# Performance work log

Measured on AMD Instinct MI355X. Metric: run time of the kernel, lower is better.

Reference implementation:

```python
import jax, jax.numpy as jnp
import numpy as np

N = 30000          # nodes
E = 480000         # edges (before self-loops)
G = 64             # graphs in batch
EMB = 64
IN = 6 + 2 * EMB   # 134
H1, C1 = 4, 128    # gat1 heads / out channels
H2, C2 = 1, 256    # gat2
LRELU_SLOPE = 0.2


def _layernorm(x, g, b, eps=1e-5):
    m = x.mean(-1, keepdims=True)
    v = ((x - m) ** 2).mean(-1, keepdims=True)
    return (x - m) / jnp.sqrt(v + eps) * g + b


def _gatv2(x, src, dst, Wl, bl, Wr, br, att, bias, H, C, n, concat):
    # GATv2 (PyG semantics, share_weights=False, eval mode -> no dropout)
    xl = (x @ Wl + bl).reshape(n, H, C)   # source transform
    xr = (x @ Wr + br).reshape(n, H, C)   # target transform
    # e_ij = att . leaky_relu(xl_j + xr_i), edges j->i : [E_tot, H]
    e = jnp.sum(jax.nn.leaky_relu(xl[src] + xr[dst], LRELU_SLOPE) * att, axis=-1)
    # scatter-softmax over incoming edges of each target node
    emax = jax.lax.stop_gradient(jax.ops.segment_max(e, dst, num_segments=n))
    ex = jnp.exp(e - emax[dst])
    den = jax.ops.segment_sum(ex, dst, num_segments=n)
    alpha = ex / (den[dst] + 1e-16)                       # [E_tot, H]
    out = jax.ops.segment_sum(alpha[:, :, None] * xl[src], dst, num_segments=n)
    if concat:
        return out.reshape(n, H * C) + bias
    return out.mean(axis=1) + bias


def setup_inputs() -> dict:
    key = jax.random.key(0)
    ks = jax.random.split(key, 24)
    s = 0.05
    inp = {
        "x_cont": jax.random.normal(ks[0], (N, 6), jnp.float32),
        "x_class": jax.random.randint(ks[1], (N,), 0, 12, jnp.int32),
        "x_pitch": jax.random.randint(ks[2], (N,), 0, 129, jnp.int32),
        "edge_index": jax.random.randint(ks[3], (2, E), 0, N, jnp.int32),
        "batch": jnp.sort(jax.random.randint(ks[4], (N,), 0, G, jnp.int32)),
        "class_tab": jax.random.normal(ks[5], (12, EMB), jnp.float32) * s,
        "pitch_tab": jax.random.normal(ks[6], (129, EMB), jnp.float32) * s,
        "Wl1": jax.random.normal(ks[7], (IN, H1 * C1), jnp.float32) * s,
        "bl1": jnp.zeros((H1 * C1,), jnp.float32),
        "Wr1": jax.random.normal(ks[8], (IN, H1 * C1), jnp.float32) * s,
        "br1": jnp.zeros((H1 * C1,), jnp.float32),
        "att1": jax.random.normal(ks[9], (H1, C1), jnp.float32) * s,
        "bias1": jnp.zeros((H1 * C1,), jnp.float32),
        "ln1_g": jnp.ones((H1 * C1,), jnp.float32),
        "ln1_b": jnp.zeros((H1 * C1,), jnp.float32),
        "Wl2": jax.random.normal(ks[10], (H1 * C1, H2 * C2), jnp.float32) * s,
        "bl2": jnp.zeros((H2 * C2,), jnp.float32),
        "Wr2": jax.random.normal(ks[11], (H1 * C1, H2 * C2), jnp.float32) * s,
        "br2": jnp.zeros((H2 * C2,), jnp.float32),
        "att2": jax.random.normal(ks[12], (H2, C2), jnp.float32) * s,
        "bias2": jnp.zeros((C2,), jnp.float32),
        "ln2_g": jnp.ones((C2,), jnp.float32),
        "ln2_b": jnp.zeros((C2,), jnp.float32),
        "Wp1": jax.random.normal(ks[13], (C2, 512), jnp.float32) * s,
        "bp1": jnp.zeros((512,), jnp.float32),
        "lnp_g": jnp.ones((512,), jnp.float32),
        "lnp_b": jnp.zeros((512,), jnp.float32),
        "Wp2": jax.random.normal(ks[14], (512, 512), jnp.float32) * s,
        "bp2": jnp.zeros((512,), jnp.float32),
    }
    return inp


def reference(x_cont, x_class, x_pitch, edge_index, batch,
              class_tab, pitch_tab,
              Wl1, bl1, Wr1, br1, att1, bias1, ln1_g, ln1_b,
              Wl2, bl2, Wr2, br2, att2, bias2, ln2_g, ln2_b,
              Wp1, bp1, lnp_g, lnp_b, Wp2, bp2):
    # node features: [N, 6 + 64 + 64]
    x = jnp.concatenate([x_cont, class_tab[x_class], pitch_tab[x_pitch]], axis=1)
    # add self-loops (PyG GATv2Conv default)
    loops = jnp.arange(N, dtype=edge_index.dtype)
    src = jnp.concatenate([edge_index[0], loops])
    dst = jnp.concatenate([edge_index[1], loops])
    x = jax.nn.elu(_layernorm(_gatv2(x, src, dst, Wl1, bl1, Wr1, br1, att1, bias1, H1, C1, N, True), ln1_g, ln1_b))
    x = jax.nn.elu(_layernorm(_gatv2(x, src, dst, Wl2, bl2, Wr2, br2, att2, bias2, H2, C2, N, False), ln2_g, ln2_b))
    # global mean pool over graphs
    sums = jax.ops.segment_sum(x, batch, num_segments=G)
    cnt = jax.ops.segment_sum(jnp.ones((N,), x.dtype), batch, num_segments=G)
    pooled = sums / jnp.maximum(cnt, 1.0)[:, None]
    # projection head + L2 normalize
    h = jax.nn.gelu(_layernorm(pooled @ Wp1 + bp1, lnp_g, lnp_b), approximate=False)
    out = h @ Wp2 + bp2
    norm = jnp.sqrt(jnp.sum(out * out, axis=1, keepdims=True))
    return out / jnp.maximum(norm, 1e-12)
```

## Files before the change

### kernel.cpp

```cpp
#include <hip/hip_runtime.h>
#include <math.h>

#define NG 64

typedef short bf16x8 __attribute__((ext_vector_type(8)));
typedef short bf16x4 __attribute__((ext_vector_type(4)));
typedef float f32x4 __attribute__((ext_vector_type(4)));

static inline int cdiv(int a, int b) { return (a + b - 1) / b; }

__device__ inline ushort f2b(float f) {
  union { float f; uint u; } v; v.f = f;
  uint u = v.u;
  return (ushort)((u + 0x7fffu + ((u >> 16) & 1u)) >> 16);
}
__device__ inline float b2f(ushort h) {
  union { uint u; float f; } v; v.u = ((uint)h) << 16;
  return v.f;
}

__global__ __launch_bounds__(256) void k_build_xb(
    const float* __restrict__ xc, const int* __restrict__ xcl,
    const int* __restrict__ xpi, const float* __restrict__ ctab,
    const float* __restrict__ ptab, ushort* __restrict__ x, int n) {
  int t = blockIdx.x * blockDim.x + threadIdx.x;
  int total = n * 160;
  if (t >= total) return;
  int node = t / 160, c = t % 160;
  float v;
  if (c < 6)        v = xc[node * 6 + c];
  else if (c < 70)  v = ctab[xcl[node] * 64 + (c - 6)];
  else if (c < 134) v = ptab[xpi[node] * 64 + (c - 70)];
  else              v = 0.f;
  x[t] = f2b(v);
}

__global__ __launch_bounds__(256) void k_prep_w1(
    const float* __restrict__ Wl, const float* __restrict__ Wr,
    ushort* __restrict__ Wt) {
  int t = blockIdx.x * blockDim.x + threadIdx.x;
  if (t >= 1024 * 160) return;
  int c = t / 160, k = t % 160;
  float v = 0.f;
  if (k < 134) v = (c < 512) ? Wl[k * 512 + c] : Wr[k * 512 + (c - 512)];
  Wt[t] = f2b(v);
}
__global__ __launch_bounds__(256) void k_prep_w2(
    const float* __restrict__ Wl, const float* __restrict__ Wr,
    ushort* __restrict__ Wt) {
  int t = blockIdx.x * blockDim.x + threadIdx.x;
  if (t >= 512 * 512) return;
  int c = t / 512, k = t % 512;
  float v = (c < 256) ? Wl[k * 256 + c] : Wr[k * 256 + (c - 256)];
  Wt[t] = f2b(v);
}

__global__ __launch_bounds__(256) void k_hist(const int* __restrict__ dst,
                                              int* __restrict__ deg, int E, int N) {
  int t = blockIdx.x * blockDim.x + threadIdx.x;
  if (t < E) atomicAdd(&deg[dst[t]], 1);
  else if (t < E + N) atomicAdd(&deg[t - E], 1);
}

__global__ __launch_bounds__(256) void k_bsum(const int* __restrict__ deg,
                                              int* __restrict__ bsum, int n) {
  int i = blockIdx.x * 256 + threadIdx.x;
  int v = (i < n) ? deg[i] : 0;
#pragma unroll
  for (int off = 1; off < 64; off <<= 1) v += __shfl_xor(v, off);
  __shared__ int ws[4];
  if ((threadIdx.x & 63) == 0) ws[threadIdx.x >> 6] = v;
  __syncthreads();
  if (threadIdx.x == 0) bsum[blockIdx.x] = ws[0] + ws[1] + ws[2] + ws[3];
}

__global__ __launch_bounds__(256) void k_scanb(const int* __restrict__ bsum,
                                               int* __restrict__ boff, int nb) {
  int t = threadIdx.x, lane = t & 63;
  int v = (t < nb) ? bsum[t] : 0;
  int incl = v;
#pragma unroll
  for (int off = 1; off < 64; off <<= 1) {
    int u = __shfl_up(incl, off);
    if (lane >= off) incl += u;
  }
  __shared__ int wsum[4];
  if (lane == 63) wsum[t >> 6] = incl;
  __syncthreads();
  int add = 0;
  for (int w = 0; w < (t >> 6); ++w) add += wsum[w];
  if (t < nb) boff[t] = incl + add - v;
}

__global__ __launch_bounds__(256) void k_scanc(const int* __restrict__ deg,
                                               const int* __restrict__ boff,
                                               int* __restrict__ rowptr, int n) {
  int b = blockIdx.x, t = threadIdx.x, lane = t & 63;
  int i = b * 256 + t;
  int v = (i < n) ? deg[i] : 0;
  int incl = v;
#pragma unroll
  for (int off = 1; off < 64; off <<= 1) {
    int u = __shfl_up(incl, off);
    if (lane >= off) incl += u;
  }
  __shared__ int wsum[4];
  if (lane == 63) wsum[t >> 6] = incl;
  __syncthreads();
  int add = boff[b];
  for (int w = 0; w < (t >> 6); ++w) add += wsum[w];
  if (i < n) rowptr[i + 1] = incl + add;
  if (i == 0) rowptr[0] = 0;
}

__global__ __launch_bounds__(256) void k_scatter(
    const int* __restrict__ src, const int* __restrict__ dst,
    const int* __restrict__ rowptr, int* __restrict__ fill,
    int* __restrict__ csr, int E, int N) {
  int t = blockIdx.x * blockDim.x + threadIdx.x;
  int s, d;
  if (t < E) { s = src[t]; d = dst[t]; }
  else if (t < E + N) { s = t - E; d = t - E; }
  else return;
  int pos = rowptr[d] + atomicAdd(&fill[d], 1);
  csr[pos] = s;
}

#define GBM 128
#define GBN 128
#define GBK 32
#define ESTRIDE 136
__device__ __forceinline__ int swzf(int r, int s) {
  return r * 64 + ((s * 16) ^ (((r >> 1) & 3) << 4));
}
__global__ __launch_bounds__(256) void k_gemm_mfma(
    const ushort* __restrict__ A, const ushort* __restrict__ Bt,
    const float* __restrict__ blo, const float* __restrict__ bhi, int nhalf,
    ushort* __restrict__ C, int M, int Kp, int NC) {
  __shared__ ushort smem[GBM * ESTRIDE];
  ushort* sA = smem;
  ushort* sB = smem + GBM * GBK;
  int tid = threadIdx.x;
  int lane = tid & 63, w = tid >> 6;
  int wr = w >> 1, wc = w & 1;
  int row0 = blockIdx.x * GBM, col0 = blockIdx.y * GBN;
  int nK = Kp / GBK;

  int rs = tid >> 2, ss = tid & 3;
  int wO0 = swzf(rs, ss);
  int wO1 = swzf(rs + 64, ss);
  bool okA0 = (row0 + rs) < M;
  bool okA1 = (row0 + rs + 64) < M;
  size_t baseA0 = (size_t)(row0 + rs) * Kp + ss * 8;
  size_t baseA1 = (size_t)(row0 + rs + 64) * Kp + ss * 8;
  size_t baseB0 = (size_t)(col0 + rs) * Kp + ss * 8;
  size_t baseB1 = (size_t)(col0 + rs + 64) * Kp + ss * 8;

  int fr = lane & 15, kq = lane >> 4;
  int aoff[4], boff[4];
#pragma unroll
  for (int m = 0; m < 4; ++m) {
    int ra = wr * 64 + m * 16 + fr;
    aoff[m] = ra * 64 + ((kq * 16) ^ (((ra >> 1) & 3) << 4));
    int rb = wc * 64 + m * 16 + fr;
    boff[m] = rb * 64 + ((kq * 16) ^ (((rb >> 1) & 3) << 4));
  }

  f32x4 acc[4][4] = {};
  bf16x8 zz = {};
  bf16x8 pa0, pa1, pb0, pb1, qa0, qa1, qb0, qb1;

#define LOADG(KS, RA0, RA1, RB0, RB1)                                   \
  do {                                                                  \
    const ushort* ap = A + (size_t)(KS) * GBK;                          \
    const ushort* bp = Bt + (size_t)(KS) * GBK;                         \
    RA0 = okA0 ? *(const bf16x8*)(ap + baseA0) : zz;                    \
    RA1 = okA1 ? *(const bf16x8*)(ap + baseA1) : zz;                    \
    RB0 = *(const bf16x8*)(bp + baseB0);                                \
    RB1 = *(const bf16x8*)(bp + baseB1);                                \
  } while (0)

#define STAGE(RA0, RA1, RB0, RB1)                                       \
  do {                                                                  \
    *(bf16x8*)((char*)sA + wO0) = RA0;                                  \
    *(bf16x8*)((char*)sA + wO1) = RA1;                                  \
    *(bf16x8*)((char*)sB + wO0) = RB0;                                  \
    *(bf16x8*)((char*)sB + wO1) = RB1;                                  \
  } while (0)

#define COMPUTE()                                                       \
  do {                                                                  \
    bf16x8 av[4], bv[4];                                                \
    _Pragma("unroll") for (int m = 0; m < 4; ++m)                       \
        av[m] = *(const bf16x8*)((const char*)sA + aoff[m]);            \
    _Pragma("unroll") for (int n = 0; n < 4; ++n)                       \
        bv[n] = *(const bf16x8*)((const char*)sB + boff[n]);            \
    _Pragma("unroll") for (int m = 0; m < 4; ++m)                       \
        _Pragma("unroll") for (int n = 0; n < 4; ++n)                   \
            acc[m][n] = __builtin_amdgcn_mfma_f32_16x16x32_bf16(        \
                av[m], bv[n], acc[m][n], 0, 0, 0);                      \
  } while (0)

  LOADG(0, pa0, pa1, pb0, pb1);
  for (int ks = 0; ks < nK; ++ks) {
    __syncthreads();
    if (ks & 1) {
      STAGE(qa0, qa1, qb0, qb1);
      if (ks + 1 < nK) LOADG(ks + 1, pa0, pa1, pb0, pb1);
    } else {
      STAGE(pa0, pa1, pb0, pb1);
      if (ks + 1 < nK) LOADG(ks + 1, qa0, qa1, qb0, qb1);
    }
    __syncthreads();
    COMPUTE();
  }

  __syncthreads();
#pragma unroll
  for (int m = 0; m < 4; ++m) {
#pragma unroll
    for (int n = 0; n < 4; ++n) {
      int tc = wc * 64 + n * 16 + fr;
      float bv = ((col0 + tc) < nhalf) ? blo[col0 + tc] : bhi[col0 + tc - nhalf];
#pragma unroll
      for (int j = 0; j < 4; ++j) {
        int tr = wr * 64 + m * 16 + kq * 4 + j;
        smem[tr * ESTRIDE + tc] = f2b(acc[m][n][j] + bv);
      }
    }
  }
  __syncthreads();
  int r0 = tid >> 4, cb = (tid & 15) * 8;
#pragma unroll
  for (int pass = 0; pass < 8; ++pass) {
    int r = pass * 16 + r0;
    int grow = row0 + r;
    if (grow < M) {
      bf16x8 vv = *(const bf16x8*)&smem[r * ESTRIDE + cb];
      *(bf16x8*)&C[(size_t)grow * NC + col0 + cb] = vv;
    }
  }
#undef LOADG
#undef STAGE
#undef COMPUTE
}

__global__ __launch_bounds__(256) void k_gat1(
    const ushort* __restrict__ xlr,
    const int* __restrict__ rowptr, const int* __restrict__ csr,
    const float* __restrict__ att, const float* __restrict__ bias,
    const float* __restrict__ lng, const float* __restrict__ lnb,
    ushort* __restrict__ out, int n) {
  int wid = (blockIdx.x * blockDim.x + threadIdx.x) >> 6;
  int lane = threadIdx.x & 63;
  if (wid >= n) return;
  int base = lane * 8;
  float xrv[8], attv[8];
  {
    bf16x8 t = *(const bf16x8*)&xlr[(size_t)wid * 1024 + 512 + base];
#pragma unroll
    for (int j = 0; j < 8; ++j) xrv[j] = b2f((ushort)t[j]);
    const float* ap = &att[base];
    float4 u0 = *(const float4*)ap;
    float4 u1 = *(const float4*)(ap + 4);
    attv[0] = u0.x; attv[1] = u0.y; attv[2] = u0.z; attv[3] = u0.w;
    attv[4] = u1.x; attv[5] = u1.y; attv[6] = u1.z; attv[7] = u1.w;
  }
  float s = 0.f;
  float acc[8] = {};
  int e0 = rowptr[wid], e1 = rowptr[wid + 1];
  bf16x8 vbn = *(const bf16x8*)&xlr[(size_t)csr[e0] * 1024 + base];
  for (int p = e0; p < e1; ++p) {
    bf16x8 vb = vbn;
    if (p + 1 < e1)
      vbn = *(const bf16x8*)&xlr[(size_t)csr[p + 1] * 1024 + base];
    float v[8];
#pragma unroll
    for (int j = 0; j < 8; ++j) v[j] = b2f((ushort)vb[j]);
    float pe = 0.f;
#pragma unroll
    for (int j = 0; j < 8; ++j) {
      float t = v[j] + xrv[j];
      t = t > 0.f ? t : 0.2f * t;
      pe += t * attv[j];
    }
    pe += __shfl_xor(pe, 1);
    pe += __shfl_xor(pe, 2);
    pe += __shfl_xor(pe, 4);
    pe += __shfl_xor(pe, 8);
    float w = __expf(pe - 8.f);
    s += w;
#pragma unroll
    for (int j = 0; j < 8; ++j) acc[j] += w * v[j];
  }
  float inv = 1.f / s;
  float o[8];
#pragma unroll
  for (int j = 0; j < 8; ++j) o[j] = acc[j] * inv + bias[base + j];
  float sum = 0.f, sq = 0.f;
#pragma unroll
  for (int j = 0; j < 8; ++j) { sum += o[j]; sq += o[j] * o[j]; }
#pragma unroll
  for (int off = 1; off < 64; off <<= 1) {
    sum += __shfl_xor(sum, off);
    sq += __shfl_xor(sq, off);
  }
  float mean = sum * (1.f / 512.f);
  float var = fmaxf(sq * (1.f / 512.f) - mean * mean, 0.f);
  float rstd = rsqrtf(var + 1e-5f);
  bf16x8 ov;
#pragma unroll
  for (int j = 0; j < 8; ++j) {
    float y = (o[j] - mean) * rstd * lng[base + j] + lnb[base + j];
    y = y > 0.f ? y : __expf(y) - 1.f;
    ov[j] = (short)f2b(y);
  }
  *(bf16x8*)&out[(size_t)wid * 512 + base] = ov;
}

__global__ __launch_bounds__(256) void k_gat2(
    const ushort* __restrict__ xlr,
    const int* __restrict__ rowptr, const int* __restrict__ csr,
    const float* __restrict__ att, const float* __restrict__ bias,
    const float* __restrict__ lng, const float* __restrict__ lnb,
    float* __restrict__ out, int n) {
  int wid = (blockIdx.x * blockDim.x + threadIdx.x) >> 6;
  int lane = threadIdx.x & 63;
  if (wid >= n) return;
  int base = lane * 4;
  float xrv[4], attv[4];
  {
    bf16x4 t = *(const bf16x4*)&xlr[(size_t)wid * 512 + 256 + base];
#pragma unroll
    for (int j = 0; j < 4; ++j) xrv[j] = b2f((ushort)t[j]);
    float4 at4 = *(const float4*)&att[base];
    attv[0] = at4.x; attv[1] = at4.y; attv[2] = at4.z; attv[3] = at4.w;
  }
  float s = 0.f;
  float acc[4] = {};
  int e0 = rowptr[wid], e1 = rowptr[wid + 1];
  bf16x4 vbn = *(const bf16x4*)&xlr[(size_t)csr[e0] * 512 + base];
  for (int p = e0; p < e1; ++p) {
    bf16x4 vb = vbn;
    if (p + 1 < e1)
      vbn = *(const bf16x4*)&xlr[(size_t)csr[p + 1] * 512 + base];
    float v[4];
#pragma unroll
    for (int j = 0; j < 4; ++j) v[j] = b2f((ushort)vb[j]);
    float pe = 0.f;
#pragma unroll
    for (int j = 0; j < 4; ++j) {
      float t = v[j] + xrv[j];
      t = t > 0.f ? t : 0.2f * t;
      pe += t * attv[j];
    }
#pragma unroll
    for (int off = 1; off < 64; off <<= 1) pe += __shfl_xor(pe, off);
    float w = __expf(pe - 8.f);
    s += w;
#pragma unroll
    for (int j = 0; j < 4; ++j) acc[j] += w * v[j];
  }
  float inv = 1.f / s;
  float o[4];
#pragma unroll
  for (int j = 0; j < 4; ++j) o[j] = acc[j] * inv + bias[base + j];
  float sum = 0.f, sq = 0.f;
#pragma unroll
  for (int j = 0; j < 4; ++j) { sum += o[j]; sq += o[j] * o[j]; }
#pragma unroll
  for (int off = 1; off < 64; off <<= 1) {
    sum += __shfl_xor(sum, off);
    sq += __shfl_xor(sq, off);
  }
  float mean = sum * (1.f / 256.f);
  float var = fmaxf(sq * (1.f / 256.f) - mean * mean, 0.f);
  float rstd = rsqrtf(var + 1e-5f);
#pragma unroll
  for (int j = 0; j < 4; ++j) {
    float y = (o[j] - mean) * rstd * lng[base + j] + lnb[base + j];
    y = y > 0.f ? y : __expf(y) - 1.f;
    out[(size_t)wid * 256 + base + j] = y;
  }
}

__global__ __launch_bounds__(256) void k_pool(
    const float* __restrict__ h2, const int* __restrict__ batch,
    float* __restrict__ pooled, int* __restrict__ cnt, int n) {
  int c = threadIdx.x;
  int n0 = blockIdx.x * 64;
  int n1 = min(n0 + 64, n);
  if (n0 >= n) return;
  float acc = 0.f;
  int cur = batch[n0];
  int cl = 0;
  for (int i = n0; i < n1; ++i) {
    int bb = batch[i];
    if (bb != cur) {
      atomicAdd(&pooled[cur * 256 + c], acc);
      if (c == 0) atomicAdd(&cnt[cur], cl);
      acc = 0.f; cl = 0; cur = bb;
    }
    acc += h2[(size_t)i * 256 + c];
    cl++;
  }
  atomicAdd(&pooled[cur * 256 + c], acc);
  if (c == 0) atomicAdd(&cnt[cur], cl);
}

__global__ __launch_bounds__(512) void k_proj1(
    const float* __restrict__ pooled, const int* __restrict__ cnt,
    const float* __restrict__ W, const float* __restrict__ b,
    const float* __restrict__ lng, const float* __restrict__ lnb,
    float* __restrict__ hout) {
  __shared__ float row[256];
  __shared__ float red[16];
  int g = blockIdx.x, c = threadIdx.x;
  if (c < 256) {
    float cc = fmaxf((float)cnt[g], 1.f);
    row[c] = pooled[g * 256 + c] / cc;
  }
  __syncthreads();
  float acc = b[c];
#pragma unroll 4
  for (int k = 0; k < 256; ++k) acc += row[k] * W[k * 512 + c];
  float sum = acc, sq = acc * acc;
#pragma unroll
  for (int off = 1; off < 64; off <<= 1) {
    sum += __shfl_xor(sum, off);
    sq += __shfl_xor(sq, off);
  }
  int wv = threadIdx.x >> 6;
  if ((threadIdx.x & 63) == 0) { red[wv] = sum; red[8 + wv] = sq; }
  __syncthreads();
  float S = 0.f, Q = 0.f;
#pragma unroll
  for (int t = 0; t < 8; ++t) { S += red[t]; Q += red[8 + t]; }
  float mean = S * (1.f / 512.f);
  float var = fmaxf(Q * (1.f / 512.f) - mean * mean, 0.f);
  float rstd = rsqrtf(var + 1e-5f);
  float y = (acc - mean) * rstd * lng[c] + lnb[c];
  float ge = 0.5f * y * (1.f + erff(y * 0.70710678118654752f));
  hout[g * 512 + c] = ge;
}

__global__ __launch_bounds__(512) void k_proj2(
    const float* __restrict__ h, const float* __restrict__ W,
    const float* __restrict__ b, float* __restrict__ out) {
  __shared__ float row[512];
  __shared__ float red[8];
  int g = blockIdx.x, c = threadIdx.x;
  row[c] = h[g * 512 + c];
  __syncthreads();
  float acc = b[c];
#pragma unroll 4
  for (int k = 0; k < 512; ++k) acc += row[k] * W[k * 512 + c];
  float sq = acc * acc;
#pragma unroll
  for (int off = 1; off < 64; off <<= 1) sq += __shfl_xor(sq, off);
  int wv = threadIdx.x >> 6;
  if ((threadIdx.x & 63) == 0) red[wv] = sq;
  __syncthreads();
  float S = 0.f;
#pragma unroll
  for (int t = 0; t < 8; ++t) S += red[t];
  float norm = fmaxf(sqrtf(S), 1e-12f);
  out[g * 512 + c] = acc / norm;
}

extern "C" void kernel_launch(void* const* d_in, const int* in_sizes, int n_in,
                              void* d_out, int out_size, void* d_ws, size_t ws_size,
                              hipStream_t stream) {
  const float* x_cont = (const float*)d_in[0];
  const int* x_class  = (const int*)d_in[1];
  const int* x_pitch  = (const int*)d_in[2];
  const int* ei       = (const int*)d_in[3];
  const int* batch    = (const int*)d_in[4];
  const float* ctab = (const float*)d_in[5];
  const float* ptab = (const float*)d_in[6];
  const float* Wl1 = (const float*)d_in[7];
  const float* bl1 = (const float*)d_in[8];
  const float* Wr1 = (const float*)d_in[9];
  const float* br1 = (const float*)d_in[10];
  const float* att1 = (const float*)d_in[11];
  const float* bias1 = (const float*)d_in[12];
  const float* ln1g = (const float*)d_in[13];
  const float* ln1b = (const float*)d_in[14];
  const float* Wl2 = (const float*)d_in[15];
  const float* bl2 = (const float*)d_in[16];
  const float* Wr2 = (const float*)d_in[17];
  const float* br2 = (const float*)d_in[18];
  const float* att2 = (const float*)d_in[19];
  const float* bias2 = (const float*)d_in[20];
  const float* ln2g = (const float*)d_in[21];
  const float* ln2b = (const float*)d_in[22];
  const float* Wp1 = (const float*)d_in[23];
  const float* bp1 = (const float*)d_in[24];
  const float* lnpg = (const float*)d_in[25];
  const float* lnpb = (const float*)d_in[26];
  const float* Wp2 = (const float*)d_in[27];
  const float* bp2 = (const float*)d_in[28];
  float* out = (float*)d_out;
  (void)n_in; (void)out_size; (void)ws_size;

  int N = in_sizes[1];
  int E = in_sizes[3] / 2;
  int ET = E + N;
  int NB = cdiv(N, 256);

  char* p = (char*)d_ws;
  ushort* xb   = (ushort*)p; p += (size_t)N * 160 * 2;
  ushort* W1t  = (ushort*)p; p += (size_t)1024 * 160 * 2;
  ushort* W2t  = (ushort*)p; p += (size_t)512 * 512 * 2;
  ushort* xlr1 = (ushort*)p; p += (size_t)N * 1024 * 2;
  ushort* h1b  = (ushort*)p; p += (size_t)N * 512 * 2;
  float* pooled = (float*)p; p += (size_t)NG * 256 * 4;
  int* cnt     = (int*)p;    p += NG * 4;
  float* hproj = (float*)p;  p += (size_t)NG * 512 * 4;
  int* deg     = (int*)p;    p += (size_t)N * 4;
  int* fill    = (int*)p;    p += (size_t)N * 4;
  int* rowptr  = (int*)p;    p += (size_t)(N + 1) * 4;
  int* csr     = (int*)p;    p += (size_t)ET * 4;
  int* bsum    = (int*)p;    p += 256 * 4;
  int* boff    = (int*)p;    p += 256 * 4;
  ushort* xlr2 = xlr1;
  float* h2   = (float*)h1b;

  const int* esrc = ei;
  const int* edst = ei + E;

  hipMemsetAsync(deg, 0, (size_t)2 * N * sizeof(int), stream);
  hipMemsetAsync(pooled, 0, (size_t)NG * 256 * sizeof(float) + NG * sizeof(int), stream);

  k_build_xb<<<cdiv(N * 160, 256), 256, 0, stream>>>(x_cont, x_class, x_pitch, ctab, ptab, xb, N);
  k_prep_w1<<<cdiv(1024 * 160, 256), 256, 0, stream>>>(Wl1, Wr1, W1t);
  k_prep_w2<<<cdiv(512 * 512, 256), 256, 0, stream>>>(Wl2, Wr2, W2t);
  k_hist<<<cdiv(ET, 256), 256, 0, stream>>>(edst, deg, E, N);
  k_bsum<<<NB, 256, 0, stream>>>(deg, bsum, N);
  k_scanb<<<1, 256, 0, stream>>>(bsum, boff, NB);
  k_scanc<<<NB, 256, 0, stream>>>(deg, boff, rowptr, N);
  k_scatter<<<cdiv(ET, 256), 256, 0, stream>>>(esrc, edst, rowptr, fill, csr, E, N);

  dim3 g1(cdiv(N, GBM), 1024 / GBN);
  k_gemm_mfma<<<g1, 256, 0, stream>>>(xb, W1t, bl1, br1, 512, xlr1, N, 160, 1024);
  k_gat1<<<cdiv(N * 64, 256), 256, 0, stream>>>(xlr1, rowptr, csr, att1, bias1, ln1g, ln1b, h1b, N);

  dim3 g2(cdiv(N, GBM), 512 / GBN);
  k_gemm_mfma<<<g2, 256, 0, stream>>>(h1b, W2t, bl2, br2, 256, xlr2, N, 512, 512);
  k_gat2<<<cdiv(N * 64, 256), 256, 0, stream>>>(xlr2, rowptr, csr, att2, bias2, ln2g, ln2b, h2, N);

  k_pool<<<cdiv(N, 64), 256, 0, stream>>>(h2, batch, pooled, cnt, N);
  k_proj1<<<NG, 512, 0, stream>>>(pooled, cnt, Wp1, bp1, lnpg, lnpb, hproj);
  k_proj2<<<NG, 512, 0, stream>>>(hproj, Wp2, bp2, out);
}
```

Measured before the change: 396.2 us.

## Batch edge gathers four-wide in GAT kernels and merge prep launches

Both GAT aggregation kernels now process incoming edges four at a time. They prefetch four neighbor rows ahead, interleave the four attention dot products and their shuffle reductions, and mask the tail edges with zero weights. Leaky-ReLU is rewritten branch-free as 0.6*t+0.4*|t|, bf16 unpacking uses bit masks, and addressing uses 32-bit byte offsets. The feature build, both weight transposes and the degree histogram are merged into one launch to cut launch overhead. The four-wide batching adds register pressure and issues redundant clamped loads at the tail of each node's edge list.

```diff
diff --git a/kernel.cpp b/kernel.cpp
--- a/kernel.cpp
+++ b/kernel.cpp
@@ -19,47 +19,65 @@
   return v.f;
 }
 
-__global__ __launch_bounds__(256) void k_build_xb(
+__device__ __forceinline__ void unpack8(bf16x8 vb, float* v) {
+  union { bf16x8 b; uint u[4]; } cv; cv.b = vb;
+#pragma unroll
+  for (int q = 0; q < 4; ++q) {
+    union { uint u; float f; } lo, hi;
+    lo.u = cv.u[q] << 16;
+    hi.u = cv.u[q] & 0xffff0000u;
+    v[2 * q] = lo.f; v[2 * q + 1] = hi.f;
+  }
+}
+__device__ __forceinline__ void unpack4(bf16x4 vb, float* v) {
+  union { bf16x4 b; uint u[2]; } cv; cv.b = vb;
+#pragma unroll
+  for (int q = 0; q < 2; ++q) {
+    union { uint u; float f; } lo, hi;
+    lo.u = cv.u[q] << 16;
+    hi.u = cv.u[q] & 0xffff0000u;
+    v[2 * q] = lo.f; v[2 * q + 1] = hi.f;
+  }
+}
+
+__global__ __launch_bounds__(256) void k_prep(
     const float* __restrict__ xc, const int* __restrict__ xcl,
     const int* __restrict__ xpi, const float* __restrict__ ctab,
-    const float* __restrict__ ptab, ushort* __restrict__ x, int n) {
+    const float* __restrict__ ptab,
+    const float* __restrict__ Wl1, const float* __restrict__ Wr1,
+    const float* __restrict__ Wl2, const float* __restrict__ Wr2,
+    const int* __restrict__ edst,
+    ushort* __restrict__ xb, ushort* __restrict__ W1t, ushort* __restrict__ W2t,
+    int* __restrict__ deg, int n, int E) {
   int t = blockIdx.x * blockDim.x + threadIdx.x;
-  int total = n * 160;
-  if (t >= total) return;
-  int node = t / 160, c = t % 160;
-  float v;
-  if (c < 6)        v = xc[node * 6 + c];
-  else if (c < 70)  v = ctab[xcl[node] * 64 + (c - 6)];
-  else if (c < 134) v = ptab[xpi[node] * 64 + (c - 70)];
-  else              v = 0.f;
-  x[t] = f2b(v);
-}
-
-__global__ __launch_bounds__(256) void k_prep_w1(
-    const float* __restrict__ Wl, const float* __restrict__ Wr,
-    ushort* __restrict__ Wt) {
-  int t = blockIdx.x * blockDim.x + threadIdx.x;
-  if (t >= 1024 * 160) return;
-  int c = t / 160, k = t % 160;
-  float v = 0.f;
-  if (k < 134) v = (c < 512) ? Wl[k * 512 + c] : Wr[k * 512 + (c - 512)];
-  Wt[t] = f2b(v);
-}
-__global__ __launch_bounds__(256) void k_prep_w2(
-    const float* __restrict__ Wl, const float* __restrict__ Wr,
-    ushort* __restrict__ Wt) {
-  int t = blockIdx.x * blockDim.x + threadIdx.x;
-  if (t >= 512 * 512) return;
-  int c = t / 512, k = t % 512;
-  float v = (c < 256) ? Wl[k * 256 + c] : Wr[k * 256 + (c - 256)];
-  Wt[t] = f2b(v);
-}
-
-__global__ __launch_bounds__(256) void k_hist(const int* __restrict__ dst,
-                                              int* __restrict__ deg, int E, int N) {
-  int t = blockIdx.x * blockDim.x + threadIdx.x;
-  if (t < E) atomicAdd(&deg[dst[t]], 1);
-  else if (t < E + N) atomicAdd(&deg[t - E], 1);
+  int T1 = n * 160;
+  int T2 = T1 + 1024 * 160;
+  int T3 = T2 + 512 * 512;
+  int T4 = T3 + E + n;
+  if (t < T1) {
+    int node = t / 160, c = t % 160;
+    float v;
+    if (c < 6)        v = xc[node * 6 + c];
+    else if (c < 70)  v = ctab[xcl[node] * 64 + (c - 6)];
+    else if (c < 134) v = ptab[xpi[node] * 64 + (c - 70)];
+    else              v = 0.f;
+    xb[t] = f2b(v);
+  } else if (t < T2) {
+    int u = t - T1;
+    int c = u / 160, k = u % 160;
+    float v = 0.f;
+    if (k < 134) v = (c < 512) ? Wl1[k * 512 + c] : Wr1[k * 512 + (c - 512)];
+    W1t[u] = f2b(v);
+  } else if (t < T3) {
+    int u = t - T2;
+    int c = u / 512, k = u % 512;
+    float v = (c < 256) ? Wl2[k * 256 + c] : Wr2[k * 256 + (c - 256)];
+    W2t[u] = f2b(v);
+  } else if (t < T4) {
+    int u = t - T3;
+    if (u < E) atomicAdd(&deg[edst[u]], 1);
+    else atomicAdd(&deg[u - E], 1);
+  }
 }
 
 __global__ __launch_bounds__(256) void k_bsum(const int* __restrict__ deg,
@@ -255,11 +273,12 @@
   int lane = threadIdx.x & 63;
   if (wid >= n) return;
   int base = lane * 8;
+  uint laneB = (uint)lane * 16u;
+  const char* xb8 = (const char*)xlr;
   float xrv[8], attv[8];
   {
-    bf16x8 t = *(const bf16x8*)&xlr[(size_t)wid * 1024 + 512 + base];
-#pragma unroll
-    for (int j = 0; j < 8; ++j) xrv[j] = b2f((ushort)t[j]);
+    bf16x8 t = *(const bf16x8*)(xb8 + ((uint)wid * 2048u + 1024u + laneB));
+    unpack8(t, xrv);
     const float* ap = &att[base];
     float4 u0 = *(const float4*)ap;
     float4 u1 = *(const float4*)(ap + 4);
@@ -269,30 +288,63 @@
   float s = 0.f;
   float acc[8] = {};
   int e0 = rowptr[wid], e1 = rowptr[wid + 1];
-  bf16x8 vbn = *(const bf16x8*)&xlr[(size_t)csr[e0] * 1024 + base];
-  for (int p = e0; p < e1; ++p) {
-    bf16x8 vb = vbn;
-    if (p + 1 < e1)
-      vbn = *(const bf16x8*)&xlr[(size_t)csr[p + 1] * 1024 + base];
-    float v[8];
-#pragma unroll
-    for (int j = 0; j < 8; ++j) v[j] = b2f((ushort)vb[j]);
-    float pe = 0.f;
+  int last = e1 - 1;
+
+#define LROW1(IDX) (*(const bf16x8*)(xb8 + (((uint)csr[IDX]) * 2048u + laneB)))
+  bf16x8 r0 = LROW1(e0);
+  bf16x8 r1 = LROW1(min(e0 + 1, last));
+  bf16x8 r2 = LROW1(min(e0 + 2, last));
+  bf16x8 r3 = LROW1(min(e0 + 3, last));
+
+  for (int pp = e0; pp < e1; pp += 4) {
+    bf16x8 c0 = r0, c1 = r1, c2 = r2, c3 = r3;
+    if (pp + 4 < e1) {
+      r0 = LROW1(pp + 4);
+      r1 = LROW1(min(pp + 5, last));
+      r2 = LROW1(min(pp + 6, last));
+      r3 = LROW1(min(pp + 7, last));
+    }
+    float v0[8], v1[8], v2[8], v3[8];
+    unpack8(c0, v0); unpack8(c1, v1); unpack8(c2, v2); unpack8(c3, v3);
+    float p1a = 0.f, p2a = 0.f, p1b = 0.f, p2b = 0.f;
+    float p1c = 0.f, p2c = 0.f, p1d = 0.f, p2d = 0.f;
 #pragma unroll
     for (int j = 0; j < 8; ++j) {
-      float t = v[j] + xrv[j];
-      t = t > 0.f ? t : 0.2f * t;
-      pe += t * attv[j];
-    }
-    pe += __shfl_xor(pe, 1);
-    pe += __shfl_xor(pe, 2);
-    pe += __shfl_xor(pe, 4);
-    pe += __shfl_xor(pe, 8);
-    float w = __expf(pe - 8.f);
-    s += w;
-#pragma unroll
-    for (int j = 0; j < 8; ++j) acc[j] += w * v[j];
-  }
+      float a = attv[j];
+      float t0 = v0[j] + xrv[j];
+      float t1 = v1[j] + xrv[j];
+      float t2 = v2[j] + xrv[j];
+      float t3 = v3[j] + xrv[j];
+      p1a = fmaf(a, t0, p1a); p2a = fmaf(a, fabsf(t0), p2a);
+      p1b = fmaf(a, t1, p1b); p2b = fmaf(a, fabsf(t1), p2b);
+      p1c = fmaf(a, t2, p1c); p2c = fmaf(a, fabsf(t2), p2c);
+      p1d = fmaf(a, t3, p1d); p2d = fmaf(a, fabsf(t3), p2d);
+    }
+    float pe0 = 0.6f * p1a + 0.4f * p2a;
+    float pe1 = 0.6f * p1b + 0.4f * p2b;
+    float pe2 = 0.6f * p1c + 0.4f * p2c;
+    float pe3 = 0.6f * p1d + 0.4f * p2d;
+#pragma unroll
+    for (int off = 1; off < 16; off <<= 1) {
+      pe0 += __shfl_xor(pe0, off);
+      pe1 += __shfl_xor(pe1, off);
+      pe2 += __shfl_xor(pe2, off);
+      pe3 += __shfl_xor(pe3, off);
+    }
+    float w0 = __expf(pe0 - 8.f);
+    float w1 = (pp + 1 <= last) ? __expf(pe1 - 8.f) : 0.f;
+    float w2 = (pp + 2 <= last) ? __expf(pe2 - 8.f) : 0.f;
+    float w3 = (pp + 3 <= last) ? __expf(pe3 - 8.f) : 0.f;
+    s += (w0 + w1) + (w2 + w3);
+#pragma unroll
+    for (int j = 0; j < 8; ++j) {
+      float t = fmaf(w0, v0[j], acc[j]);
+      t = fmaf(w1, v1[j], t);
+      t = fmaf(w2, v2[j], t);
+      acc[j] = fmaf(w3, v3[j], t);
+    }
+  }
+#undef LROW1
   float inv = 1.f / s;
   float o[8];
 #pragma unroll
@@ -328,39 +380,75 @@
   int lane = threadIdx.x & 63;
   if (wid >= n) return;
   int base = lane * 4;
+  uint laneB = (uint)lane * 8u;
+  const char* xb8 = (const char*)xlr;
   float xrv[4], attv[4];
   {
-    bf16x4 t = *(const bf16x4*)&xlr[(size_t)wid * 512 + 256 + base];
-#pragma unroll
-    for (int j = 0; j < 4; ++j) xrv[j] = b2f((ushort)t[j]);
+    bf16x4 t = *(const bf16x4*)(xb8 + ((uint)wid * 1024u + 512u + laneB));
+    unpack4(t, xrv);
     float4 at4 = *(const float4*)&att[base];
     attv[0] = at4.x; attv[1] = at4.y; attv[2] = at4.z; attv[3] = at4.w;
   }
   float s = 0.f;
   float acc[4] = {};
   int e0 = rowptr[wid], e1 = rowptr[wid + 1];
-  bf16x4 vbn = *(const bf16x4*)&xlr[(size_t)csr[e0] * 512 + base];
-  for (int p = e0; p < e1; ++p) {
-    bf16x4 vb = vbn;
-    if (p + 1 < e1)
-      vbn = *(const bf16x4*)&xlr[(size_t)csr[p + 1] * 512 + base];
-    float v[4];
-#pragma unroll
-    for (int j = 0; j < 4; ++j) v[j] = b2f((ushort)vb[j]);
-    float pe = 0.f;
+  int last = e1 - 1;
+
+#define LROW2(IDX) (*(const bf16x4*)(xb8 + (((uint)csr[IDX]) * 1024u + laneB)))
+  bf16x4 r0 = LROW2(e0);
+  bf16x4 r1 = LROW2(min(e0 + 1, last));
+  bf16x4 r2 = LROW2(min(e0 + 2, last));
+  bf16x4 r3 = LROW2(min(e0 + 3, last));
+
+  for (int pp = e0; pp < e1; pp += 4) {
+    bf16x4 c0 = r0, c1 = r1, c2 = r2, c3 = r3;
+    if (pp + 4 < e1) {
+      r0 = LROW2(pp + 4);
+      r1 = LROW2(min(pp + 5, last));
+      r2 = LROW2(min(pp + 6, last));
+      r3 = LROW2(min(pp + 7, last));
+    }
+    float v0[4], v1[4], v2[4], v3[4];
+    unpack4(c0, v0); unpack4(c1, v1); unpack4(c2, v2); unpack4(c3, v3);
+    float p1a = 0.f, p2a = 0.f, p1b = 0.f, p2b = 0.f;
+    float p1c = 0.f, p2c = 0.f, p1d = 0.f, p2d = 0.f;
 #pragma unroll
     for (int j = 0; j < 4; ++j) {
-      float t = v[j] + xrv[j];
-      t = t > 0.f ? t : 0.2f * t;
-      pe += t * attv[j];
-    }
-#pragma unroll
-    for (int off = 1; off < 64; off <<= 1) pe += __shfl_xor(pe, off);
-    float w = __expf(pe - 8.f);
-    s += w;
-#pragma unroll
-    for (int j = 0; j < 4; ++j) acc[j] += w * v[j];
-  }
+      float a = attv[j];
+      float t0 = v0[j] + xrv[j];
+      float t1 = v1[j] + xrv[j];
+      float t2 = v2[j] + xrv[j];
+      float t3 = v3[j] + xrv[j];
+      p1a = fmaf(a, t0, p1a); p2a = fmaf(a, fabsf(t0), p2a);
+      p1b = fmaf(a, t1, p1b); p2b = fmaf(a, fabsf(t1), p2b);
+      p1c = fmaf(a, t2, p1c); p2c = fmaf(a, fabsf(t2), p2c);
+      p1d = fmaf(a, t3, p1d); p2d = fmaf(a, fabsf(t3), p2d);
+    }
+    float pe0 = 0.6f * p1a + 0.4f * p2a;
+    float pe1 = 0.6f * p1b + 0.4f * p2b;
+    float pe2 = 0.6f * p1c + 0.4f * p2c;
+    float pe3 = 0.6f * p1d + 0.4f * p2d;
+#pragma unroll
+    for (int off = 1; off < 64; off <<= 1) {
+      pe0 += __shfl_xor(pe0, off);
+      pe1 += __shfl_xor(pe1, off);
+      pe2 += __shfl_xor(pe2, off);
+      pe3 += __shfl_xor(pe3, off);
+    }
+    float w0 = __expf(pe0 - 8.f);
+    float w1 = (pp + 1 <= last) ? __expf(pe1 - 8.f) : 0.f;
+    float w2 = (pp + 2 <= last) ? __expf(pe2 - 8.f) : 0.f;
+    float w3 = (pp + 3 <= last) ? __expf(pe3 - 8.f) : 0.f;
+    s += (w0 + w1) + (w2 + w3);
+#pragma unroll
+    for (int j = 0; j < 4; ++j) {
+      float t = fmaf(w0, v0[j], acc[j]);
+      t = fmaf(w1, v1[j], t);
+      t = fmaf(w2, v2[j], t);
+      acc[j] = fmaf(w3, v3[j], t);
+    }
+  }
+#undef LROW2
   float inv = 1.f / s;
   float o[4];
 #pragma unroll
@@ -532,10 +620,10 @@
   hipMemsetAsync(deg, 0, (size_t)2 * N * sizeof(int), stream);
   hipMemsetAsync(pooled, 0, (size_t)NG * 256 * sizeof(float) + NG * sizeof(int), stream);
 
-  k_build_xb<<<cdiv(N * 160, 256), 256, 0, stream>>>(x_cont, x_class, x_pitch, ctab, ptab, xb, N);
-  k_prep_w1<<<cdiv(1024 * 160, 256), 256, 0, stream>>>(Wl1, Wr1, W1t);
-  k_prep_w2<<<cdiv(512 * 512, 256), 256, 0, stream>>>(Wl2, Wr2, W2t);
-  k_hist<<<cdiv(ET, 256), 256, 0, stream>>>(edst, deg, E, N);
+  int prep_total = N * 160 + 1024 * 160 + 512 * 512 + ET;
+  k_prep<<<cdiv(prep_total, 256), 256, 0, stream>>>(
+      x_cont, x_class, x_pitch, ctab, ptab, Wl1, Wr1, Wl2, Wr2, edst,
+      xb, W1t, W2t, deg, N, E);
   k_bsum<<<NB, 256, 0, stream>>>(deg, bsum, N);
   k_scanb<<<1, 256, 0, stream>>>(bsum, boff, NB);
   k_scanc<<<NB, 256, 0, stream>>>(deg, boff, rowptr, N);
```

Measured after the change: 348.6 us. -12.0%, faster.
